# Performance work log

Hardware: AMD Instinct MI355X
Metric: run time of the kernel (lower is better)

## Reference

```python
import jax, jax.numpy as jnp
import numpy as np

TOPK = 2
ALPHA = 0.1
EPS = 1e-20


def setup_inputs() -> dict:
    key = jax.random.key(0)
    k1, k2 = jax.random.split(key)
    hidden_states = jax.random.normal(k1, (4, 4096, 2048), dtype=jnp.float32)
    # kaiming_uniform_(a=sqrt(5)) on [E, H] ~ U(-1/sqrt(H), 1/sqrt(H))
    bound = 1.0 / np.sqrt(2048)
    weight = jax.random.uniform(k2, (64, 2048), dtype=jnp.float32, minval=-bound, maxval=bound)
    return {"hidden_states": hidden_states, "weight": weight}


def reference(hidden_states, weight):
    B, S, H = hidden_states.shape
    E = weight.shape[0]
    x = hidden_states.reshape(-1, H)                      # [B*S, H]
    logits = jnp.einsum('th,eh->te', x, weight)           # [B*S, E]
    scores = jax.nn.softmax(logits, axis=-1)
    topk_weight, topk_idx = jax.lax.top_k(scores, TOPK)   # [B*S, K]
    # norm_topk_prob
    topk_weight = topk_weight / (topk_weight.sum(axis=-1, keepdims=True) + EPS)
    # seq_aux load-balancing loss (training path)
    idx = topk_idx.reshape(B, S * TOPK)                   # [B, S*K]
    ce = jnp.zeros((B, E), dtype=scores.dtype)
    ce = ce.at[jnp.arange(B)[:, None], idx].add(1.0)      # scatter_add counts
    ce = ce * (E / (S * TOPK))
    expert_scores = scores.reshape(B, S, E).mean(axis=1)  # [B, E]
    aux_loss = (ce * expert_scores).sum(axis=1).mean() * ALPHA
    return topk_idx, topk_weight, aux_loss
```

## Files before the change

### kernel.cpp

```cpp
#include <hip/hip_runtime.h>

#define TAU 8e-3f

typedef __attribute__((ext_vector_type(8))) short bf16x8;
typedef __attribute__((ext_vector_type(4))) float f32x4;

#define ACCUM_OFF 262144

#define RNE16(f) \
  ((unsigned short)((__float_as_uint(f) + 0x7fffu + ((__float_as_uint(f) >> 16) & 1u)) >> 16))

__global__ __launch_bounds__(256) void wconv(const float* __restrict__ W,
                                             unsigned short* __restrict__ Wswz,
                                             float* __restrict__ accum) {
  int t = blockIdx.x * 256 + threadIdx.x;
  int g = t >> 12, rem = t & 4095;
  int ks = rem >> 6, lane = rem & 63;
  int fm = lane & 15, kg = lane >> 4;
  const float* src = W + (size_t)(g * 16 + fm) * 2048 + ks * 32 + kg * 8;
  float4 a = *(const float4*)src;
  float4 b = *(const float4*)(src + 4);
  ushort4 lo = make_ushort4(RNE16(a.x), RNE16(a.y), RNE16(a.z), RNE16(a.w));
  ushort4 hi = make_ushort4(RNE16(b.x), RNE16(b.y), RNE16(b.z), RNE16(b.w));
  unsigned short* dst = Wswz + (size_t)t * 8;
  *(ushort4*)dst = lo;
  *(ushort4*)(dst + 4) = hi;
  if (blockIdx.x == 0) {
    accum[threadIdx.x] = 0.f;
    accum[256 + threadIdx.x] = 0.f;
    if (threadIdx.x == 0) ((unsigned*)accum)[512] = 0u;
  }
}

#define CVT8(d, p0, p1)              \
  {                                  \
    d[0] = (short)RNE16(p0.x);       \
    d[1] = (short)RNE16(p0.y);       \
    d[2] = (short)RNE16(p0.z);       \
    d[3] = (short)RNE16(p0.w);       \
    d[4] = (short)RNE16(p1.x);       \
    d[5] = (short)RNE16(p1.y);       \
    d[6] = (short)RNE16(p1.z);       \
    d[7] = (short)RNE16(p1.w);       \
  }

__global__ __launch_bounds__(512, 4) void gate_main(
    const float* __restrict__ x, const float* __restrict__ Wf,
    const unsigned short* __restrict__ Wswz,
    float* __restrict__ out, float* __restrict__ accum) {
  __shared__ float part[8][32][68];
  __shared__ float m2s[32], m1s[32], izs[32];
  __shared__ int i1s[32], i2s[32];

  const int tid = threadIdx.x;
  const int lane = tid & 63;
  const int w = __builtin_amdgcn_readfirstlane(tid >> 6);
  const int fm = lane & 15;
  const int kg = lane >> 4;
  const int tok0 = blockIdx.x * 32;

  const float* xr0 = x + (size_t)(tok0 + fm) * 2048 + w * 256 + kg * 8;
  const float* xr1 = xr0 + (size_t)16 * 2048;
  const bf16x8* wsw = (const bf16x8*)Wswz + lane;

  f32x4 acc[2][4];
#pragma unroll
  for (int f = 0; f < 2; ++f)
#pragma unroll
    for (int g = 0; g < 4; ++g) acc[f][g] = (f32x4){0.f, 0.f, 0.f, 0.f};

#pragma unroll
  for (int it = 0; it < 8; ++it) {
    const int ks = w * 8 + it;
    float4 p0 = *(const float4*)(xr0 + it * 32);
    float4 p1 = *(const float4*)(xr0 + it * 32 + 4);
    float4 q0 = *(const float4*)(xr1 + it * 32);
    float4 q1 = *(const float4*)(xr1 + it * 32 + 4);
    bf16x8 b0 = wsw[(0 * 64 + ks) * 64];
    bf16x8 b1 = wsw[(1 * 64 + ks) * 64];
    bf16x8 b2 = wsw[(2 * 64 + ks) * 64];
    bf16x8 b3 = wsw[(3 * 64 + ks) * 64];
    bf16x8 a0, a1;
    CVT8(a0, p0, p1)
    CVT8(a1, q0, q1)
    acc[0][0] = __builtin_amdgcn_mfma_f32_16x16x32_bf16(a0, b0, acc[0][0], 0, 0, 0);
    acc[0][1] = __builtin_amdgcn_mfma_f32_16x16x32_bf16(a0, b1, acc[0][1], 0, 0, 0);
    acc[0][2] = __builtin_amdgcn_mfma_f32_16x16x32_bf16(a0, b2, acc[0][2], 0, 0, 0);
    acc[0][3] = __builtin_amdgcn_mfma_f32_16x16x32_bf16(a0, b3, acc[0][3], 0, 0, 0);
    acc[1][0] = __builtin_amdgcn_mfma_f32_16x16x32_bf16(a1, b0, acc[1][0], 0, 0, 0);
    acc[1][1] = __builtin_amdgcn_mfma_f32_16x16x32_bf16(a1, b1, acc[1][1], 0, 0, 0);
    acc[1][2] = __builtin_amdgcn_mfma_f32_16x16x32_bf16(a1, b2, acc[1][2], 0, 0, 0);
    acc[1][3] = __builtin_amdgcn_mfma_f32_16x16x32_bf16(a1, b3, acc[1][3], 0, 0, 0);
  }

#pragma unroll
  for (int f = 0; f < 2; ++f)
#pragma unroll
    for (int g = 0; g < 4; ++g)
#pragma unroll
      for (int r = 0; r < 4; ++r)
        part[w][f * 16 + kg * 4 + r][g * 16 + fm] = acc[f][g][r];
  __syncthreads();

#pragma unroll
  for (int p = tid; p < 2048; p += 512) {
    int t = p >> 6, e = p & 63;
    float s = part[0][t][e];
#pragma unroll
    for (int ww = 1; ww < 8; ++ww) s += part[ww][t][e];
    part[0][t][e] = s;
  }
  __syncthreads();

  if (w != 0) return;

  const int t = lane;
  float m1 = -3e38f, m2 = -3e38f, m3 = -3e38f;
  int i1 = 0, i2 = 0;
  if (lane < 32) {
    for (int e = 0; e < 64; ++e) {
      float v = part[0][t][e];
      if (v > m1) { m3 = m2; m2 = m1; i2 = i1; m1 = v; i1 = e; }
      else if (v > m2) { m3 = m2; m2 = v; i2 = e; }
      else if (v > m3) { m3 = v; }
    }
    m2s[t] = m2;
  }
  bool flg = (lane < 32) && ((m1 - m2 < TAU) || (m2 - m3 < TAU));
  unsigned long long msk = __ballot(flg);

  while (msk) {
    int tt = __ffsll(msk) - 1;
    msk &= msk - 1;
    float thr = m2s[tt] - TAU;
    unsigned long long cand = __ballot(part[0][tt][lane] >= thr);
    const float* xr = x + (size_t)(tok0 + tt) * 2048 + lane * 32;
    while (cand) {
      int e = __ffsll(cand) - 1;
      cand &= cand - 1;
      const float* wr = Wf + (size_t)e * 2048 + lane * 32;
      float s = 0.f;
#pragma unroll
      for (int kk = 0; kk < 32; kk += 8) {
        float4 u0 = *(const float4*)(xr + kk);
        float4 v0 = *(const float4*)(wr + kk);
        float4 u1 = *(const float4*)(xr + kk + 4);
        float4 v1 = *(const float4*)(wr + kk + 4);
        s += u0.x * v0.x + u0.y * v0.y + u0.z * v0.z + u0.w * v0.w +
             u1.x * v1.x + u1.y * v1.y + u1.z * v1.z + u1.w * v1.w;
      }
      for (int o = 32; o; o >>= 1) s += __shfl_xor(s, o, 64);
      if (lane == 0) part[0][tt][e] = s;
    }
  }

  if (lane < 32) {
    m1 = -3e38f; m2 = -3e38f; i1 = 0; i2 = 0;
    for (int e = 0; e < 64; ++e) {
      float v = part[0][t][e];
      if (v > m1) { m2 = m1; i2 = i1; m1 = v; i1 = e; }
      else if (v > m2) { m2 = v; i2 = e; }
    }
    float Z = 0.f;
    for (int e = 0; e < 64; ++e) Z += __expf(part[0][t][e] - m1);
    float iz = 1.f / Z;
    float p1 = iz;
    float p2 = __expf(m2 - m1) * iz;
    float dn = 1.f / (p1 + p2 + 1e-20f);
    size_t tg = (size_t)(tok0 + t);
    out[tg * 2 + 0] = (float)i1;
    out[tg * 2 + 1] = (float)i2;
    out[32768 + tg * 2 + 0] = p1 * dn;
    out[32768 + tg * 2 + 1] = p2 * dn;
    m1s[t] = m1; izs[t] = iz; i1s[t] = i1; i2s[t] = i2;
  }

  const int b = blockIdx.x >> 7;
  float ssum = 0.f;
  int cnt = 0;
#pragma unroll
  for (int t2 = 0; t2 < 32; ++t2) {
    ssum += __expf(part[0][t2][lane] - m1s[t2]) * izs[t2];
    cnt += (i1s[t2] == lane) + (i2s[t2] == lane);
  }
  atomicAdd(&accum[b * 64 + lane], ssum);
  atomicAdd(&accum[256 + b * 64 + lane], (float)cnt);

  __threadfence();
  unsigned old = 0;
  if (lane == 0) old = atomicAdd((unsigned*)accum + 512, 1u);
  old = (unsigned)__shfl((int)old, 0, 64);
  if (old == 511u) {
    __threadfence();
    float tot = 0.f;
#pragma unroll
    for (int bb = 0; bb < 4; ++bb) {
      float ss = atomicAdd(&accum[bb * 64 + lane], 0.f);
      float cc = atomicAdd(&accum[256 + bb * 64 + lane], 0.f);
      tot += cc * (1.f / 128.f) * (ss * (1.f / 4096.f));
    }
    for (int o = 32; o; o >>= 1) tot += __shfl_xor(tot, o, 64);
    if (lane == 0) out[65536] = 0.025f * tot;
  }
}

extern "C" void kernel_launch(void* const* d_in, const int* in_sizes, int n_in,
                              void* d_out, int out_size, void* d_ws, size_t ws_size,
                              hipStream_t stream) {
  const float* x = (const float*)d_in[0];
  const float* Wf = (const float*)d_in[1];
  float* out = (float*)d_out;
  unsigned short* Wswz = (unsigned short*)d_ws;
  float* accum = (float*)((char*)d_ws + ACCUM_OFF);
  wconv<<<64, 256, 0, stream>>>(Wf, Wswz, accum);
  gate_main<<<512, 512, 0, stream>>>(x, Wf, Wswz, out, accum);
}
```

Before: 224.7 us.

## Restructure gate GEMM into 16-token wave pairs with register double-buffered loads

Each block now covers 64 tokens split into four 16-token groups. Each group is handled by a pair of waves that split K in halves, and each wave loops over 32 K-steps with software-prefetched x and weight registers. The cross-wave LDS reduction over 8 partials is replaced by a two-way add, and the conversion to bf16 uses the packed v_cvt_pk_bf16_f32 instruction. The aim is to hide global load latency, cut LDS traffic and synchronisation, and use cheaper conversions. In exchange there are fewer blocks (256) and lower occupancy, and four waves per block now do the top-k and aux epilogue in parallel.

```diff
diff --git a/kernel.cpp b/kernel.cpp
--- a/kernel.cpp
+++ b/kernel.cpp
@@ -4,6 +4,7 @@
 
 typedef __attribute__((ext_vector_type(8))) short bf16x8;
 typedef __attribute__((ext_vector_type(4))) float f32x4;
+typedef __attribute__((ext_vector_type(4))) unsigned int u32x4;
 
 #define ACCUM_OFF 262144
 
@@ -32,109 +33,108 @@
   }
 }
 
-#define CVT8(d, p0, p1)              \
-  {                                  \
-    d[0] = (short)RNE16(p0.x);       \
-    d[1] = (short)RNE16(p0.y);       \
-    d[2] = (short)RNE16(p0.z);       \
-    d[3] = (short)RNE16(p0.w);       \
-    d[4] = (short)RNE16(p1.x);       \
-    d[5] = (short)RNE16(p1.y);       \
-    d[6] = (short)RNE16(p1.z);       \
-    d[7] = (short)RNE16(p1.w);       \
-  }
-
-__global__ __launch_bounds__(512, 4) void gate_main(
+#define CVTPK(dst, a, b) \
+  asm("v_cvt_pk_bf16_f32 %0, %1, %2" : "=v"(dst) : "v"(a), "v"(b))
+
+__global__ __launch_bounds__(512, 2) void gate_main(
     const float* __restrict__ x, const float* __restrict__ Wf,
     const unsigned short* __restrict__ Wswz,
     float* __restrict__ out, float* __restrict__ accum) {
-  __shared__ float part[8][32][68];
-  __shared__ float m2s[32], m1s[32], izs[32];
-  __shared__ int i1s[32], i2s[32];
+  __shared__ float part[4][16][68];
 
   const int tid = threadIdx.x;
   const int lane = tid & 63;
   const int w = __builtin_amdgcn_readfirstlane(tid >> 6);
+  const int p = w >> 1;
+  const int h = w & 1;
   const int fm = lane & 15;
   const int kg = lane >> 4;
-  const int tok0 = blockIdx.x * 32;
-
-  const float* xr0 = x + (size_t)(tok0 + fm) * 2048 + w * 256 + kg * 8;
-  const float* xr1 = xr0 + (size_t)16 * 2048;
+  const int tokp = blockIdx.x * 64 + p * 16;
+
+  const float* xr = x + (size_t)(tokp + fm) * 2048 + h * 1024 + kg * 8;
   const bf16x8* wsw = (const bf16x8*)Wswz + lane;
-
-  f32x4 acc[2][4];
-#pragma unroll
-  for (int f = 0; f < 2; ++f)
-#pragma unroll
-    for (int g = 0; g < 4; ++g) acc[f][g] = (f32x4){0.f, 0.f, 0.f, 0.f};
-
-#pragma unroll
-  for (int it = 0; it < 8; ++it) {
-    const int ks = w * 8 + it;
-    float4 p0 = *(const float4*)(xr0 + it * 32);
-    float4 p1 = *(const float4*)(xr0 + it * 32 + 4);
-    float4 q0 = *(const float4*)(xr1 + it * 32);
-    float4 q1 = *(const float4*)(xr1 + it * 32 + 4);
-    bf16x8 b0 = wsw[(0 * 64 + ks) * 64];
-    bf16x8 b1 = wsw[(1 * 64 + ks) * 64];
-    bf16x8 b2 = wsw[(2 * 64 + ks) * 64];
-    bf16x8 b3 = wsw[(3 * 64 + ks) * 64];
-    bf16x8 a0, a1;
-    CVT8(a0, p0, p1)
-    CVT8(a1, q0, q1)
-    acc[0][0] = __builtin_amdgcn_mfma_f32_16x16x32_bf16(a0, b0, acc[0][0], 0, 0, 0);
-    acc[0][1] = __builtin_amdgcn_mfma_f32_16x16x32_bf16(a0, b1, acc[0][1], 0, 0, 0);
-    acc[0][2] = __builtin_amdgcn_mfma_f32_16x16x32_bf16(a0, b2, acc[0][2], 0, 0, 0);
-    acc[0][3] = __builtin_amdgcn_mfma_f32_16x16x32_bf16(a0, b3, acc[0][3], 0, 0, 0);
-    acc[1][0] = __builtin_amdgcn_mfma_f32_16x16x32_bf16(a1, b0, acc[1][0], 0, 0, 0);
-    acc[1][1] = __builtin_amdgcn_mfma_f32_16x16x32_bf16(a1, b1, acc[1][1], 0, 0, 0);
-    acc[1][2] = __builtin_amdgcn_mfma_f32_16x16x32_bf16(a1, b2, acc[1][2], 0, 0, 0);
-    acc[1][3] = __builtin_amdgcn_mfma_f32_16x16x32_bf16(a1, b3, acc[1][3], 0, 0, 0);
-  }
-
-#pragma unroll
-  for (int f = 0; f < 2; ++f)
+  const int ks0 = h * 32;
+
+  f32x4 acc[4];
+#pragma unroll
+  for (int g = 0; g < 4; ++g) acc[g] = (f32x4){0.f, 0.f, 0.f, 0.f};
+
+  float4 xa0 = *(const float4*)(xr);
+  float4 xa1 = *(const float4*)(xr + 4);
+  float4 xb0 = *(const float4*)(xr + 32);
+  float4 xb1 = *(const float4*)(xr + 36);
+  bf16x8 w0 = wsw[(0 * 64 + ks0) * 64];
+  bf16x8 w1 = wsw[(1 * 64 + ks0) * 64];
+  bf16x8 w2 = wsw[(2 * 64 + ks0) * 64];
+  bf16x8 w3 = wsw[(3 * 64 + ks0) * 64];
+
+#pragma unroll
+  for (int it = 0; it < 32; ++it) {
+    float4 xn0 = {}, xn1 = {};
+    bf16x8 n0 = {}, n1 = {}, n2 = {}, n3 = {};
+    if (it < 30) {
+      xn0 = *(const float4*)(xr + (it + 2) * 32);
+      xn1 = *(const float4*)(xr + (it + 2) * 32 + 4);
+    }
+    if (it < 31) {
+      const int ks = ks0 + it + 1;
+      n0 = wsw[(0 * 64 + ks) * 64];
+      n1 = wsw[(1 * 64 + ks) * 64];
+      n2 = wsw[(2 * 64 + ks) * 64];
+      n3 = wsw[(3 * 64 + ks) * 64];
+    }
+    unsigned u0, u1, u2, u3;
+    CVTPK(u0, xa0.x, xa0.y);
+    CVTPK(u1, xa0.z, xa0.w);
+    CVTPK(u2, xa1.x, xa1.y);
+    CVTPK(u3, xa1.z, xa1.w);
+    u32x4 uu = (u32x4){u0, u1, u2, u3};
+    bf16x8 a = __builtin_bit_cast(bf16x8, uu);
+    acc[0] = __builtin_amdgcn_mfma_f32_16x16x32_bf16(a, w0, acc[0], 0, 0, 0);
+    acc[1] = __builtin_amdgcn_mfma_f32_16x16x32_bf16(a, w1, acc[1], 0, 0, 0);
+    acc[2] = __builtin_amdgcn_mfma_f32_16x16x32_bf16(a, w2, acc[2], 0, 0, 0);
+    acc[3] = __builtin_amdgcn_mfma_f32_16x16x32_bf16(a, w3, acc[3], 0, 0, 0);
+    xa0 = xb0; xa1 = xb1; xb0 = xn0; xb1 = xn1;
+    w0 = n0; w1 = n1; w2 = n2; w3 = n3;
+  }
+
+  if (h) {
 #pragma unroll
     for (int g = 0; g < 4; ++g)
 #pragma unroll
       for (int r = 0; r < 4; ++r)
-        part[w][f * 16 + kg * 4 + r][g * 16 + fm] = acc[f][g][r];
+        part[p][kg * 4 + r][g * 16 + fm] = acc[g][r];
+  }
   __syncthreads();
-
-#pragma unroll
-  for (int p = tid; p < 2048; p += 512) {
-    int t = p >> 6, e = p & 63;
-    float s = part[0][t][e];
-#pragma unroll
-    for (int ww = 1; ww < 8; ++ww) s += part[ww][t][e];
-    part[0][t][e] = s;
-  }
-  __syncthreads();
-
-  if (w != 0) return;
+  if (h) return;
+
+#pragma unroll
+  for (int g = 0; g < 4; ++g)
+#pragma unroll
+    for (int r = 0; r < 4; ++r)
+      part[p][kg * 4 + r][g * 16 + fm] += acc[g][r];
 
   const int t = lane;
   float m1 = -3e38f, m2 = -3e38f, m3 = -3e38f;
   int i1 = 0, i2 = 0;
-  if (lane < 32) {
+  if (lane < 16) {
     for (int e = 0; e < 64; ++e) {
-      float v = part[0][t][e];
+      float v = part[p][t][e];
       if (v > m1) { m3 = m2; m2 = m1; i2 = i1; m1 = v; i1 = e; }
       else if (v > m2) { m3 = m2; m2 = v; i2 = e; }
       else if (v > m3) { m3 = v; }
     }
-    m2s[t] = m2;
-  }
-  bool flg = (lane < 32) && ((m1 - m2 < TAU) || (m2 - m3 < TAU));
+    part[p][t][64] = m2;
+  }
+  bool flg = (lane < 16) && ((m1 - m2 < TAU) || (m2 - m3 < TAU));
   unsigned long long msk = __ballot(flg);
 
   while (msk) {
     int tt = __ffsll(msk) - 1;
     msk &= msk - 1;
-    float thr = m2s[tt] - TAU;
-    unsigned long long cand = __ballot(part[0][tt][lane] >= thr);
-    const float* xr = x + (size_t)(tok0 + tt) * 2048 + lane * 32;
+    float thr = part[p][tt][64] - TAU;
+    unsigned long long cand = __ballot(part[p][tt][lane] >= thr);
+    const float* xr2 = x + (size_t)(tokp + tt) * 2048 + lane * 32;
     while (cand) {
       int e = __ffsll(cand) - 1;
       cand &= cand - 1;
@@ -142,46 +142,53 @@
       float s = 0.f;
 #pragma unroll
       for (int kk = 0; kk < 32; kk += 8) {
-        float4 u0 = *(const float4*)(xr + kk);
-        float4 v0 = *(const float4*)(wr + kk);
-        float4 u1 = *(const float4*)(xr + kk + 4);
-        float4 v1 = *(const float4*)(wr + kk + 4);
-        s += u0.x * v0.x + u0.y * v0.y + u0.z * v0.z + u0.w * v0.w +
-             u1.x * v1.x + u1.y * v1.y + u1.z * v1.z + u1.w * v1.w;
+        float4 uu0 = *(const float4*)(xr2 + kk);
+        float4 vv0 = *(const float4*)(wr + kk);
+        float4 uu1 = *(const float4*)(xr2 + kk + 4);
+        float4 vv1 = *(const float4*)(wr + kk + 4);
+        s += uu0.x * vv0.x + uu0.y * vv0.y + uu0.z * vv0.z + uu0.w * vv0.w +
+             uu1.x * vv1.x + uu1.y * vv1.y + uu1.z * vv1.z + uu1.w * vv1.w;
       }
       for (int o = 32; o; o >>= 1) s += __shfl_xor(s, o, 64);
-      if (lane == 0) part[0][tt][e] = s;
-    }
-  }
-
-  if (lane < 32) {
+      if (lane == 0) part[p][tt][e] = s;
+    }
+  }
+
+  if (lane < 16) {
     m1 = -3e38f; m2 = -3e38f; i1 = 0; i2 = 0;
     for (int e = 0; e < 64; ++e) {
-      float v = part[0][t][e];
+      float v = part[p][t][e];
       if (v > m1) { m2 = m1; i2 = i1; m1 = v; i1 = e; }
       else if (v > m2) { m2 = v; i2 = e; }
     }
     float Z = 0.f;
-    for (int e = 0; e < 64; ++e) Z += __expf(part[0][t][e] - m1);
+    for (int e = 0; e < 64; ++e) Z += __expf(part[p][t][e] - m1);
     float iz = 1.f / Z;
     float p1 = iz;
     float p2 = __expf(m2 - m1) * iz;
     float dn = 1.f / (p1 + p2 + 1e-20f);
-    size_t tg = (size_t)(tok0 + t);
+    size_t tg = (size_t)(tokp + t);
     out[tg * 2 + 0] = (float)i1;
     out[tg * 2 + 1] = (float)i2;
     out[32768 + tg * 2 + 0] = p1 * dn;
     out[32768 + tg * 2 + 1] = p2 * dn;
-    m1s[t] = m1; izs[t] = iz; i1s[t] = i1; i2s[t] = i2;
-  }
-
-  const int b = blockIdx.x >> 7;
+    part[p][t][64] = m1;
+    part[p][t][65] = iz;
+    part[p][t][66] = __int_as_float(i1);
+    part[p][t][67] = __int_as_float(i2);
+  }
+
+  const int b = blockIdx.x >> 6;
   float ssum = 0.f;
   int cnt = 0;
 #pragma unroll
-  for (int t2 = 0; t2 < 32; ++t2) {
-    ssum += __expf(part[0][t2][lane] - m1s[t2]) * izs[t2];
-    cnt += (i1s[t2] == lane) + (i2s[t2] == lane);
+  for (int t2 = 0; t2 < 16; ++t2) {
+    float m1t = part[p][t2][64];
+    float izt = part[p][t2][65];
+    int i1t = __float_as_int(part[p][t2][66]);
+    int i2t = __float_as_int(part[p][t2][67]);
+    ssum += __expf(part[p][t2][lane] - m1t) * izt;
+    cnt += (i1t == lane) + (i2t == lane);
   }
   atomicAdd(&accum[b * 64 + lane], ssum);
   atomicAdd(&accum[256 + b * 64 + lane], (float)cnt);
@@ -190,7 +197,7 @@
   unsigned old = 0;
   if (lane == 0) old = atomicAdd((unsigned*)accum + 512, 1u);
   old = (unsigned)__shfl((int)old, 0, 64);
-  if (old == 511u) {
+  if (old == 1023u) {
     __threadfence();
     float tot = 0.f;
 #pragma unroll
@@ -213,5 +220,5 @@
   unsigned short* Wswz = (unsigned short*)d_ws;
   float* accum = (float*)((char*)d_ws + ACCUM_OFF);
   wconv<<<64, 256, 0, stream>>>(Wf, Wswz, accum);
-  gate_main<<<512, 512, 0, stream>>>(x, Wf, Wswz, out, accum);
+  gate_main<<<256, 512, 0, stream>>>(x, Wf, Wswz, out, accum);
 }
```

After: 245.2 us. 9.1% more time.

## Split gating into GEMM kernel and wave-parallel top-k/softmax kernel

Applied to the files above, without the earlier changes.

Splits the fused kernel in two. A GEMM kernel uses 16-token tiles, 1024 blocks and higher occupancy, and writes fp32 logits to workspace. A second kernel does top-k, softmax, exact fp32 recheck of near-ties and aux-loss accumulation with one wavefront per token, using shuffle reductions instead of a serial single-wave loop. It also swaps the manual RNE bf16 conversion for the packed v_cvt_pk_bf16_f32 instruction. The cost is an extra launch and a round trip of logits through global memory, but it removes the serial tail where only one wave per block worked.

```diff
diff --git a/kernel.cpp b/kernel.cpp
--- a/kernel.cpp
+++ b/kernel.cpp
@@ -4,11 +4,16 @@
 
 typedef __attribute__((ext_vector_type(8))) short bf16x8;
 typedef __attribute__((ext_vector_type(4))) float f32x4;
-
-#define ACCUM_OFF 262144
+typedef __attribute__((ext_vector_type(4))) unsigned int u32x4;
+
+#define LOGITS_OFF 262144
+#define ACCUM_OFF (262144 + 4194304)
 
 #define RNE16(f) \
   ((unsigned short)((__float_as_uint(f) + 0x7fffu + ((__float_as_uint(f) >> 16) & 1u)) >> 16))
+
+#define CVTPK(dst, a, b) \
+  asm("v_cvt_pk_bf16_f32 %0, %1, %2" : "=v"(dst) : "v"(a), "v"(b))
 
 __global__ __launch_bounds__(256) void wconv(const float* __restrict__ W,
                                              unsigned short* __restrict__ Wswz,
@@ -32,175 +37,188 @@
   }
 }
 
-#define CVT8(d, p0, p1)              \
-  {                                  \
-    d[0] = (short)RNE16(p0.x);       \
-    d[1] = (short)RNE16(p0.y);       \
-    d[2] = (short)RNE16(p0.z);       \
-    d[3] = (short)RNE16(p0.w);       \
-    d[4] = (short)RNE16(p1.x);       \
-    d[5] = (short)RNE16(p1.y);       \
-    d[6] = (short)RNE16(p1.z);       \
-    d[7] = (short)RNE16(p1.w);       \
-  }
-
-__global__ __launch_bounds__(512, 4) void gate_main(
-    const float* __restrict__ x, const float* __restrict__ Wf,
-    const unsigned short* __restrict__ Wswz,
-    float* __restrict__ out, float* __restrict__ accum) {
-  __shared__ float part[8][32][68];
-  __shared__ float m2s[32], m1s[32], izs[32];
-  __shared__ int i1s[32], i2s[32];
+__global__ __launch_bounds__(512, 8) void gate_gemm(
+    const float* __restrict__ x, const unsigned short* __restrict__ Wswz,
+    float* __restrict__ logits) {
+  __shared__ float part[8][16][68];
 
   const int tid = threadIdx.x;
   const int lane = tid & 63;
   const int w = __builtin_amdgcn_readfirstlane(tid >> 6);
   const int fm = lane & 15;
   const int kg = lane >> 4;
-  const int tok0 = blockIdx.x * 32;
-
-  const float* xr0 = x + (size_t)(tok0 + fm) * 2048 + w * 256 + kg * 8;
-  const float* xr1 = xr0 + (size_t)16 * 2048;
+  const int tok0 = blockIdx.x * 16;
+
+  const float* xr = x + (size_t)(tok0 + fm) * 2048 + w * 256 + kg * 8;
   const bf16x8* wsw = (const bf16x8*)Wswz + lane;
 
-  f32x4 acc[2][4];
-#pragma unroll
-  for (int f = 0; f < 2; ++f)
-#pragma unroll
-    for (int g = 0; g < 4; ++g) acc[f][g] = (f32x4){0.f, 0.f, 0.f, 0.f};
+  f32x4 acc[4];
+#pragma unroll
+  for (int g = 0; g < 4; ++g) acc[g] = (f32x4){0.f, 0.f, 0.f, 0.f};
 
 #pragma unroll
   for (int it = 0; it < 8; ++it) {
     const int ks = w * 8 + it;
-    float4 p0 = *(const float4*)(xr0 + it * 32);
-    float4 p1 = *(const float4*)(xr0 + it * 32 + 4);
-    float4 q0 = *(const float4*)(xr1 + it * 32);
-    float4 q1 = *(const float4*)(xr1 + it * 32 + 4);
+    float4 p0 = *(const float4*)(xr + it * 32);
+    float4 p1 = *(const float4*)(xr + it * 32 + 4);
     bf16x8 b0 = wsw[(0 * 64 + ks) * 64];
     bf16x8 b1 = wsw[(1 * 64 + ks) * 64];
     bf16x8 b2 = wsw[(2 * 64 + ks) * 64];
     bf16x8 b3 = wsw[(3 * 64 + ks) * 64];
-    bf16x8 a0, a1;
-    CVT8(a0, p0, p1)
-    CVT8(a1, q0, q1)
-    acc[0][0] = __builtin_amdgcn_mfma_f32_16x16x32_bf16(a0, b0, acc[0][0], 0, 0, 0);
-    acc[0][1] = __builtin_amdgcn_mfma_f32_16x16x32_bf16(a0, b1, acc[0][1], 0, 0, 0);
-    acc[0][2] = __builtin_amdgcn_mfma_f32_16x16x32_bf16(a0, b2, acc[0][2], 0, 0, 0);
-    acc[0][3] = __builtin_amdgcn_mfma_f32_16x16x32_bf16(a0, b3, acc[0][3], 0, 0, 0);
-    acc[1][0] = __builtin_amdgcn_mfma_f32_16x16x32_bf16(a1, b0, acc[1][0], 0, 0, 0);
-    acc[1][1] = __builtin_amdgcn_mfma_f32_16x16x32_bf16(a1, b1, acc[1][1], 0, 0, 0);
-    acc[1][2] = __builtin_amdgcn_mfma_f32_16x16x32_bf16(a1, b2, acc[1][2], 0, 0, 0);
-    acc[1][3] = __builtin_amdgcn_mfma_f32_16x16x32_bf16(a1, b3, acc[1][3], 0, 0, 0);
-  }
-
-#pragma unroll
-  for (int f = 0; f < 2; ++f)
-#pragma unroll
-    for (int g = 0; g < 4; ++g)
-#pragma unroll
-      for (int r = 0; r < 4; ++r)
-        part[w][f * 16 + kg * 4 + r][g * 16 + fm] = acc[f][g][r];
+    unsigned u0, u1, u2, u3;
+    CVTPK(u0, p0.x, p0.y);
+    CVTPK(u1, p0.z, p0.w);
+    CVTPK(u2, p1.x, p1.y);
+    CVTPK(u3, p1.z, p1.w);
+    u32x4 uu = (u32x4){u0, u1, u2, u3};
+    bf16x8 a = __builtin_bit_cast(bf16x8, uu);
+    acc[0] = __builtin_amdgcn_mfma_f32_16x16x32_bf16(a, b0, acc[0], 0, 0, 0);
+    acc[1] = __builtin_amdgcn_mfma_f32_16x16x32_bf16(a, b1, acc[1], 0, 0, 0);
+    acc[2] = __builtin_amdgcn_mfma_f32_16x16x32_bf16(a, b2, acc[2], 0, 0, 0);
+    acc[3] = __builtin_amdgcn_mfma_f32_16x16x32_bf16(a, b3, acc[3], 0, 0, 0);
+  }
+
+#pragma unroll
+  for (int g = 0; g < 4; ++g)
+#pragma unroll
+    for (int r = 0; r < 4; ++r)
+      part[w][kg * 4 + r][g * 16 + fm] = acc[g][r];
   __syncthreads();
 
 #pragma unroll
-  for (int p = tid; p < 2048; p += 512) {
+  for (int p = tid; p < 1024; p += 512) {
     int t = p >> 6, e = p & 63;
     float s = part[0][t][e];
 #pragma unroll
     for (int ww = 1; ww < 8; ++ww) s += part[ww][t][e];
-    part[0][t][e] = s;
-  }
-  __syncthreads();
-
-  if (w != 0) return;
-
-  const int t = lane;
-  float m1 = -3e38f, m2 = -3e38f, m3 = -3e38f;
-  int i1 = 0, i2 = 0;
-  if (lane < 32) {
-    for (int e = 0; e < 64; ++e) {
-      float v = part[0][t][e];
-      if (v > m1) { m3 = m2; m2 = m1; i2 = i1; m1 = v; i1 = e; }
-      else if (v > m2) { m3 = m2; m2 = v; i2 = e; }
-      else if (v > m3) { m3 = v; }
-    }
-    m2s[t] = m2;
-  }
-  bool flg = (lane < 32) && ((m1 - m2 < TAU) || (m2 - m3 < TAU));
-  unsigned long long msk = __ballot(flg);
-
-  while (msk) {
-    int tt = __ffsll(msk) - 1;
-    msk &= msk - 1;
-    float thr = m2s[tt] - TAU;
-    unsigned long long cand = __ballot(part[0][tt][lane] >= thr);
-    const float* xr = x + (size_t)(tok0 + tt) * 2048 + lane * 32;
-    while (cand) {
-      int e = __ffsll(cand) - 1;
-      cand &= cand - 1;
-      const float* wr = Wf + (size_t)e * 2048 + lane * 32;
-      float s = 0.f;
-#pragma unroll
-      for (int kk = 0; kk < 32; kk += 8) {
-        float4 u0 = *(const float4*)(xr + kk);
-        float4 v0 = *(const float4*)(wr + kk);
-        float4 u1 = *(const float4*)(xr + kk + 4);
-        float4 v1 = *(const float4*)(wr + kk + 4);
-        s += u0.x * v0.x + u0.y * v0.y + u0.z * v0.z + u0.w * v0.w +
-             u1.x * v1.x + u1.y * v1.y + u1.z * v1.z + u1.w * v1.w;
-      }
-      for (int o = 32; o; o >>= 1) s += __shfl_xor(s, o, 64);
-      if (lane == 0) part[0][tt][e] = s;
-    }
-  }
-
-  if (lane < 32) {
-    m1 = -3e38f; m2 = -3e38f; i1 = 0; i2 = 0;
-    for (int e = 0; e < 64; ++e) {
-      float v = part[0][t][e];
-      if (v > m1) { m2 = m1; i2 = i1; m1 = v; i1 = e; }
-      else if (v > m2) { m2 = v; i2 = e; }
-    }
-    float Z = 0.f;
-    for (int e = 0; e < 64; ++e) Z += __expf(part[0][t][e] - m1);
+    logits[(size_t)(tok0 + t) * 64 + e] = s;
+  }
+}
+
+__global__ __launch_bounds__(1024) void gate_top(
+    const float* __restrict__ x, const float* __restrict__ Wf,
+    const float* __restrict__ logits, float* __restrict__ out,
+    float* __restrict__ accum) {
+  __shared__ float sm[16][64];
+  __shared__ float cn[16][64];
+
+  const int tid = threadIdx.x;
+  const int lane = tid & 63;
+  const int w = tid >> 6;
+  const int tok0 = blockIdx.x * 64;
+  const int b = blockIdx.x >> 6;
+
+  float ssum = 0.f;
+  float cnt = 0.f;
+
+  for (int i = 0; i < 4; ++i) {
+    const int tok = tok0 + w * 4 + i;
+    float v = logits[(size_t)tok * 64 + lane];
+
+    float m1 = v; int i1 = lane;
+#pragma unroll
+    for (int o = 32; o; o >>= 1) {
+      float ov = __shfl_xor(m1, o, 64);
+      int oi = __shfl_xor(i1, o, 64);
+      if (ov > m1 || (ov == m1 && oi < i1)) { m1 = ov; i1 = oi; }
+    }
+    float v2 = (lane == i1) ? -3e38f : v;
+    float m2 = v2; int i2 = lane;
+#pragma unroll
+    for (int o = 32; o; o >>= 1) {
+      float ov = __shfl_xor(m2, o, 64);
+      int oi = __shfl_xor(i2, o, 64);
+      if (ov > m2 || (ov == m2 && oi < i2)) { m2 = ov; i2 = oi; }
+    }
+    float m3 = (lane == i1 || lane == i2) ? -3e38f : v;
+#pragma unroll
+    for (int o = 32; o; o >>= 1) m3 = fmaxf(m3, __shfl_xor(m3, o, 64));
+
+    if ((m1 - m2 < TAU) || (m2 - m3 < TAU)) {
+      unsigned long long cand = __ballot(v >= m2 - TAU);
+      const float* xr2 = x + (size_t)tok * 2048 + lane * 32;
+      while (cand) {
+        int e = __ffsll(cand) - 1;
+        cand &= cand - 1;
+        const float* wr = Wf + (size_t)e * 2048 + lane * 32;
+        float s = 0.f;
+#pragma unroll
+        for (int kk = 0; kk < 32; kk += 8) {
+          float4 u0 = *(const float4*)(xr2 + kk);
+          float4 w0 = *(const float4*)(wr + kk);
+          float4 u1 = *(const float4*)(xr2 + kk + 4);
+          float4 w1 = *(const float4*)(wr + kk + 4);
+          s += u0.x * w0.x + u0.y * w0.y + u0.z * w0.z + u0.w * w0.w +
+               u1.x * w1.x + u1.y * w1.y + u1.z * w1.z + u1.w * w1.w;
+        }
+#pragma unroll
+        for (int o = 32; o; o >>= 1) s += __shfl_xor(s, o, 64);
+        if (lane == e) v = s;
+      }
+      m1 = v; i1 = lane;
+#pragma unroll
+      for (int o = 32; o; o >>= 1) {
+        float ov = __shfl_xor(m1, o, 64);
+        int oi = __shfl_xor(i1, o, 64);
+        if (ov > m1 || (ov == m1 && oi < i1)) { m1 = ov; i1 = oi; }
+      }
+      v2 = (lane == i1) ? -3e38f : v;
+      m2 = v2; i2 = lane;
+#pragma unroll
+      for (int o = 32; o; o >>= 1) {
+        float ov = __shfl_xor(m2, o, 64);
+        int oi = __shfl_xor(i2, o, 64);
+        if (ov > m2 || (ov == m2 && oi < i2)) { m2 = ov; i2 = oi; }
+      }
+    }
+
+    float ez = __expf(v - m1);
+    float Z = ez;
+#pragma unroll
+    for (int o = 32; o; o >>= 1) Z += __shfl_xor(Z, o, 64);
     float iz = 1.f / Z;
     float p1 = iz;
     float p2 = __expf(m2 - m1) * iz;
     float dn = 1.f / (p1 + p2 + 1e-20f);
-    size_t tg = (size_t)(tok0 + t);
-    out[tg * 2 + 0] = (float)i1;
-    out[tg * 2 + 1] = (float)i2;
-    out[32768 + tg * 2 + 0] = p1 * dn;
-    out[32768 + tg * 2 + 1] = p2 * dn;
-    m1s[t] = m1; izs[t] = iz; i1s[t] = i1; i2s[t] = i2;
-  }
-
-  const int b = blockIdx.x >> 7;
-  float ssum = 0.f;
-  int cnt = 0;
-#pragma unroll
-  for (int t2 = 0; t2 < 32; ++t2) {
-    ssum += __expf(part[0][t2][lane] - m1s[t2]) * izs[t2];
-    cnt += (i1s[t2] == lane) + (i2s[t2] == lane);
-  }
-  atomicAdd(&accum[b * 64 + lane], ssum);
-  atomicAdd(&accum[256 + b * 64 + lane], (float)cnt);
-
-  __threadfence();
-  unsigned old = 0;
-  if (lane == 0) old = atomicAdd((unsigned*)accum + 512, 1u);
-  old = (unsigned)__shfl((int)old, 0, 64);
-  if (old == 511u) {
+    if (lane == 0) {
+      size_t tg = (size_t)tok;
+      out[tg * 2 + 0] = (float)i1;
+      out[tg * 2 + 1] = (float)i2;
+      out[32768 + tg * 2 + 0] = p1 * dn;
+      out[32768 + tg * 2 + 1] = p2 * dn;
+    }
+    ssum += ez * iz;
+    cnt += (float)((lane == i1) + (lane == i2));
+  }
+
+  sm[w][lane] = ssum;
+  cn[w][lane] = cnt;
+  __syncthreads();
+
+  if (tid < 64) {
+    float s = 0.f, c = 0.f;
+#pragma unroll
+    for (int ww = 0; ww < 16; ++ww) { s += sm[ww][tid]; c += cn[ww][tid]; }
+    atomicAdd(&accum[b * 64 + tid], s);
+    atomicAdd(&accum[256 + b * 64 + tid], c);
+
     __threadfence();
-    float tot = 0.f;
-#pragma unroll
-    for (int bb = 0; bb < 4; ++bb) {
-      float ss = atomicAdd(&accum[bb * 64 + lane], 0.f);
-      float cc = atomicAdd(&accum[256 + bb * 64 + lane], 0.f);
-      tot += cc * (1.f / 128.f) * (ss * (1.f / 4096.f));
-    }
-    for (int o = 32; o; o >>= 1) tot += __shfl_xor(tot, o, 64);
-    if (lane == 0) out[65536] = 0.025f * tot;
+    unsigned old = 0;
+    if (tid == 0) old = atomicAdd((unsigned*)accum + 512, 1u);
+    old = (unsigned)__shfl((int)old, 0, 64);
+    if (old == 255u) {
+      __threadfence();
+      float tot = 0.f;
+#pragma unroll
+      for (int bb = 0; bb < 4; ++bb) {
+        float ss = atomicAdd(&accum[bb * 64 + tid], 0.f);
+        float cc = atomicAdd(&accum[256 + bb * 64 + tid], 0.f);
+        tot += cc * (1.f / 128.f) * (ss * (1.f / 4096.f));
+      }
+#pragma unroll
+      for (int o = 32; o; o >>= 1) tot += __shfl_xor(tot, o, 64);
+      if (tid == 0) out[65536] = 0.025f * tot;
+    }
   }
 }
 
@@ -211,7 +229,9 @@
   const float* Wf = (const float*)d_in[1];
   float* out = (float*)d_out;
   unsigned short* Wswz = (unsigned short*)d_ws;
+  float* logits = (float*)((char*)d_ws + LOGITS_OFF);
   float* accum = (float*)((char*)d_ws + ACCUM_OFF);
   wconv<<<64, 256, 0, stream>>>(Wf, Wswz, accum);
-  gate_main<<<512, 512, 0, stream>>>(x, Wf, Wswz, out, accum);
-}
+  gate_gemm<<<1024, 512, 0, stream>>>(x, Wswz, logits);
+  gate_top<<<256, 1024, 0, stream>>>(x, Wf, logits, out, accum);
+}
```

Result: no change. 221.7 us (-1.4%).
